# Kernel optimization log

Hardware: AMD Instinct MI355X
Metric: run time of the kernel (lower is better)

## Reference

```python
import jax, jax.numpy as jnp
import numpy as np

N, S, C, G = 40000, 16, 96, 12
EPS = 1e-5

def ln(x, g, b):
    mu = jnp.mean(x, -1, keepdims=True)
    var = jnp.mean((x - mu) ** 2, -1, keepdims=True)
    return (x - mu) * jax.lax.rsqrt(var + EPS) * g + b

def setup_inputs() -> dict:
    key = jax.random.key(0)
    ks = jax.random.split(key, 20)
    s = 0.05
    inp = {
        'q': jax.random.normal(ks[0], (N, C), jnp.float32),
        'k': jax.random.normal(ks[1], (N, C), jnp.float32),
        'v': jax.random.normal(ks[2], (N, C), jnp.float32),
        'xyz': jax.random.normal(ks[3], (N, 3), jnp.float32),
        'reference_index': jax.random.randint(ks[4], (N, S), 0, N, jnp.int32),
        # linear_q: Linear(C,C)+LN(C)+ReLU
        'Wq': jax.random.normal(ks[5], (C, C), jnp.float32) * s,
        'bq': jnp.zeros((C,), jnp.float32),
        'gq': jnp.ones((C,), jnp.float32),
        'betaq': jnp.zeros((C,), jnp.float32),
        # linear_k
        'Wk': jax.random.normal(ks[6], (C, C), jnp.float32) * s,
        'bk': jnp.zeros((C,), jnp.float32),
        'gk': jnp.ones((C,), jnp.float32),
        'betak': jnp.zeros((C,), jnp.float32),
        # linear_v
        'Wv': jax.random.normal(ks[7], (C, C), jnp.float32) * s,
        'bv': jnp.zeros((C,), jnp.float32),
        # linear_p_bias: Linear(3,C)+LN(C)+ReLU+Linear(C,C)
        'Wp1': jax.random.normal(ks[8], (3, C), jnp.float32) * s,
        'bp1': jnp.zeros((C,), jnp.float32),
        'gp': jnp.ones((C,), jnp.float32),
        'betap': jnp.zeros((C,), jnp.float32),
        'Wp2': jax.random.normal(ks[9], (C, C), jnp.float32) * s,
        'bp2': jnp.zeros((C,), jnp.float32),
        # weight_encoding: Linear(C,G)+LN(G)+ReLU+Linear(G,G)
        'Ww1': jax.random.normal(ks[10], (C, G), jnp.float32) * s,
        'bw1': jnp.zeros((G,), jnp.float32),
        'gw': jnp.ones((G,), jnp.float32),
        'betaw': jnp.zeros((G,), jnp.float32),
        'Ww2': jax.random.normal(ks[11], (G, G), jnp.float32) * s,
        'bw2': jnp.zeros((G,), jnp.float32),
    }
    return inp

def reference(q, k, v, xyz, reference_index,
              Wq, bq, gq, betaq, Wk, bk, gk, betak, Wv, bv,
              Wp1, bp1, gp, betap, Wp2, bp2,
              Ww1, bw1, gw, betaw, Ww2, bw2):
    query = jax.nn.relu(ln(q @ Wq + bq, gq, betaq))            # [N, C]
    keyf  = jax.nn.relu(ln(k @ Wk + bk, gk, betak))            # [N, C]
    val   = v @ Wv + bv                                        # [N, C]

    idx = reference_index                                      # [N, S]
    mask = (idx >= 0).astype(q.dtype)                          # sign(idx+1)
    safe = jnp.clip(idx, 0, None)
    # pointops.grouping: gather w/ zero-fill at idx=-1; with_xyz prepends relative coords
    pos  = (xyz[safe] - xyz[:, None, :]) * mask[..., None]     # [N, S, 3]
    keyg = keyf[safe] * mask[..., None]                        # [N, S, C]
    valg = val[safe] * mask[..., None]                         # [N, S, C]

    rel = keyg - query[:, None, :]                             # [N, S, C]
    peb = jax.nn.relu(ln(pos @ Wp1 + bp1, gp, betap)) @ Wp2 + bp2
    rel = rel + peb
    valg = valg + peb

    w = jax.nn.relu(ln(rel @ Ww1 + bw1, gw, betaw)) @ Ww2 + bw2  # [N, S, G]
    w = jax.nn.softmax(w, axis=1) * mask[..., None]              # softmax over neighbors

    valg = valg.reshape(N, S, G, C // G)
    feat = jnp.einsum('nsgi,nsg->ngi', valg, w).reshape(N, C)
    return feat
```

## Files before the change

kernel.cpp:

```cpp
#include <hip/hip_runtime.h>

#define NN 40000
#define SS 16
#define CC 96
#define GG 12
#define SXP 104

typedef __attribute__((ext_vector_type(8))) short bf16x8;
typedef __attribute__((ext_vector_type(4))) float f32x4;

__device__ __forceinline__ short f2bf(float f) {
    union { float f; unsigned u; } c; c.f = f;
    unsigned r = (c.u + 0x7fffu + ((c.u >> 16) & 1u)) >> 16;
    return (short)r;
}
__device__ __forceinline__ unsigned pack2bf(float hi, float lo) {
    unsigned a = __float_as_uint(hi) + 0x8000u;
    unsigned b = __float_as_uint(lo) + 0x8000u;
    return __builtin_amdgcn_perm(a, b, 0x07060302u);
}
__device__ __forceinline__ ushort f2bf_hu(float f) {
    return (ushort)((__float_as_uint(f) + 0x8000u) >> 16);
}
__device__ __forceinline__ float bf2f(ushort u) {
    return __uint_as_float(((unsigned)u) << 16);
}

template<int CTRL>
__device__ __forceinline__ float dppf(float x) {
    int r = __builtin_amdgcn_mov_dpp(__float_as_int(x), CTRL, 0xF, 0xF, true);
    return __int_as_float(r);
}
__device__ __forceinline__ float row16_sum(float x) {
    x += dppf<0xB1>(x);
    x += dppf<0x4E>(x);
    x += dppf<0x141>(x);
    x += dppf<0x140>(x);
    return x;
}
__device__ __forceinline__ float row16_max(float x) {
    x = fmaxf(x, dppf<0xB1>(x));
    x = fmaxf(x, dppf<0x4E>(x));
    x = fmaxf(x, dppf<0x141>(x));
    x = fmaxf(x, dppf<0x140>(x));
    return x;
}

#define J_W3   27648
#define J_P2   (J_W3 + 9216)
#define J_W1   (J_P2 + 1536)
#define J_WF   (J_W1 + 1536)
#define J_CF   (J_WF + 12)
#define J_S4   (J_CF + 4)
#define J_G    (J_S4 + 16)

__global__ void prep_kernel(const float* __restrict__ Wq, const float* __restrict__ Wk,
                            const float* __restrict__ Wv, const float* __restrict__ Wp2,
                            const float* __restrict__ Ww1, const float* __restrict__ bp2,
                            const float* __restrict__ bw1, const float* __restrict__ Wp1,
                            const float* __restrict__ bp1,
                            ushort* __restrict__ fragQKV, ushort* __restrict__ fragP2,
                            ushort* __restrict__ fragW1, ushort* __restrict__ fragWf,
                            float* __restrict__ cfused, float* __restrict__ stats)
{
    const int job = blockIdx.x*256 + threadIdx.x;
    if (job < J_W3) {
        const int which = job / 9216, o = job % 9216;
        const float* W = (which == 0) ? Wq : (which == 1) ? Wk : Wv;
        const int pos = o >> 3, j = o & 7;
        const int lane = pos & 63, ntkb = pos >> 6;
        const int nt = ntkb / 3, kb = ntkb - nt*3;
        const int col = nt*16 + (lane & 15), krow = kb*32 + (lane >> 4)*8 + j;
        fragQKV[job] = (ushort)f2bf(W[krow*CC + col]);
    } else if (job < J_P2) {
        const int o = job - J_W3;
        const int pos = o >> 3, j = o & 7;
        const int lane = pos & 63, ntkb = pos >> 6;
        const int nt = ntkb / 3, kb = ntkb - nt*3;
        const int col = nt*16 + (lane & 15), krow = kb*32 + (lane >> 4)*8 + j;
        fragP2[o] = (ushort)f2bf(Wp2[krow*CC + col]);
    } else if (job < J_W1) {
        const int o = job - J_P2;
        const int pos = o >> 3, j = o & 7;
        const int lane = pos & 63, kb = pos >> 6;
        const int col = lane & 15, krow = kb*32 + (lane >> 4)*8 + j;
        fragW1[o] = (col < GG) ? (ushort)f2bf(Ww1[krow*GG + col]) : (ushort)0;
    } else if (job < J_WF) {
        const int o = job - J_W1;
        const int pos = o >> 3, j = o & 7;
        const int lane = pos & 63, kb = pos >> 6;
        const int col = lane & 15, krow = kb*32 + (lane >> 4)*8 + j;
        float s = 0.f;
        if (col < GG) for (int jj = 0; jj < CC; ++jj) s += Wp2[krow*CC + jj] * Ww1[jj*GG + col];
        fragWf[o] = (col < GG) ? (ushort)f2bf(s) : (ushort)0;
    } else if (job < J_CF) {
        const int g = job - J_WF;
        float s = bw1[g];
        for (int jj = 0; jj < CC; ++jj) s += bp2[jj] * Ww1[jj*GG + g];
        cfused[g] = s;
    } else if (job < J_S4) {
        const int d = job - J_CF;
        float s = 0.f;
        for (int c = 0; c < CC; ++c) s += (d < 3) ? Wp1[d*CC + c] : bp1[c];
        stats[d] = s;
    } else if (job < J_G) {
        const int o = job - J_S4, d1 = o >> 2, d2 = o & 3;
        float s = 0.f;
        for (int c = 0; c < CC; ++c) {
            const float a1 = (d1 < 3) ? Wp1[d1*CC + c] : bp1[c];
            const float a2 = (d2 < 3) ? Wp1[d2*CC + c] : bp1[c];
            s += a1*a2;
        }
        stats[4 + o] = s;
    }
}

__global__ __launch_bounds__(256) void qkv_mfma(
    const float* __restrict__ q, const float* __restrict__ kx, const float* __restrict__ v,
    const float* __restrict__ bq, const float* __restrict__ gq, const float* __restrict__ betaq,
    const float* __restrict__ bk, const float* __restrict__ gk, const float* __restrict__ betak,
    const float* __restrict__ bv,
    const ushort* __restrict__ fragQKV, const ushort* __restrict__ fragW1,
    ushort* __restrict__ valout, float* __restrict__ qw1out, float* __restrict__ kw1out)
{
    __shared__ float sbias[CC], sg[CC], sbeta[CC];
    __shared__ __align__(16) ushort sx2[4][16*SXP];

    const int p = blockIdx.y;
    const float* X; const float* b;
    const float* g = nullptr; const float* beta = nullptr;
    if (p == 0)      { X = q;  b = bq; g = gq; beta = betaq; }
    else if (p == 1) { X = kx; b = bk; g = gk; beta = betak; }
    else             { X = v;  b = bv; }
    const bool has_ln = (p < 2);
    float* w1out = (p == 0) ? qw1out : kw1out;

    const int t = threadIdx.x;
    if (t < CC) {
        sbias[t] = b[t];
        if (has_ln) { sg[t] = g[t]; sbeta[t] = beta[t]; }
    }

    const int lane = t & 63, w = t >> 6;
    const int c16 = lane & 15, quad = lane >> 4;
    const ushort* fragW = fragQKV + p*9216;

    bf16x8 Ww1f[3];
    if (has_ln) {
        #pragma unroll
        for (int kb = 0; kb < 3; ++kb) {
            union { bf16x8 v; uint4 u; } wu;
            wu.u = ((const uint4*)fragW1)[kb*64 + lane];
            Ww1f[kb] = wu.v;
        }
    }

    __syncthreads();

    const f32x4 zero4 = {0.f, 0.f, 0.f, 0.f};
    ushort* sxw = sx2[w];
    const int tile = blockIdx.x*4 + w;
    const int row0 = tile * 16;

    const float* xr = X + (size_t)(row0 + c16)*CC;
    bf16x8 Af[3];
    #pragma unroll
    for (int kb = 0; kb < 3; ++kb) {
        const float4 a0 = *(const float4*)(xr + kb*32 + quad*8);
        const float4 a1 = *(const float4*)(xr + kb*32 + quad*8 + 4);
        union { bf16x8 v; uint u[4]; } au;
        au.u[0] = pack2bf(a0.y, a0.x);
        au.u[1] = pack2bf(a0.w, a0.z);
        au.u[2] = pack2bf(a1.y, a1.x);
        au.u[3] = pack2bf(a1.w, a1.z);
        Af[kb] = au.v;
    }

    f32x4 acc[6];
    #pragma unroll
    for (int nt = 0; nt < 6; ++nt) acc[nt] = zero4;
    #pragma unroll
    for (int kb = 0; kb < 3; ++kb)
        #pragma unroll
        for (int nt = 0; nt < 6; ++nt) {
            const bf16x8 bf = *(const bf16x8*)(fragW + ((nt*3 + kb)*64 + lane)*8);
            acc[nt] = __builtin_amdgcn_mfma_f32_16x16x32_bf16(Af[kb], bf, acc[nt], 0, 0, 0);
        }

    #pragma unroll
    for (int nt = 0; nt < 6; ++nt) {
        const float bb = sbias[nt*16 + c16];
        #pragma unroll
        for (int r = 0; r < 4; ++r) acc[nt][r] += bb;
    }

    if (has_ln) {
        #pragma unroll
        for (int r = 0; r < 4; ++r) {
            float sum = 0.f, sq = 0.f;
            #pragma unroll
            for (int nt = 0; nt < 6; ++nt) { float x = acc[nt][r]; sum += x; sq += x*x; }
            sum = row16_sum(sum); sq = row16_sum(sq);
            const float mu  = sum * (1.f/96.f);
            const float var = sq * (1.f/96.f) - mu*mu;
            const float rs  = rsqrtf(var + 1e-5f);
            #pragma unroll
            for (int nt = 0; nt < 6; ++nt) {
                const int c = nt*16 + c16;
                acc[nt][r] = fmaxf((acc[nt][r] - mu)*rs*sg[c] + sbeta[c], 0.f);
            }
        }
        #pragma unroll
        for (int nt = 0; nt < 6; ++nt)
            #pragma unroll
            for (int r = 0; r < 4; ++r)
                sxw[(quad*4 + r)*SXP + nt*16 + c16] = f2bf_hu(acc[nt][r]);

        f32x4 o = zero4;
        #pragma unroll
        for (int kb = 0; kb < 3; ++kb) {
            const bf16x8 aA = *(const bf16x8*)(sxw + c16*SXP + kb*32 + quad*8);
            o = __builtin_amdgcn_mfma_f32_16x16x32_bf16(aA, Ww1f[kb], o, 0, 0, 0);
        }
        if (c16 < GG) {
            #pragma unroll
            for (int r = 0; r < 4; ++r)
                w1out[(size_t)(row0 + quad*4 + r)*GG + c16] = o[r];
        }
    } else {
        #pragma unroll
        for (int r = 0; r < 4; ++r)
            #pragma unroll
            for (int nt = 0; nt < 6; ++nt)
                valout[(size_t)(row0 + quad*4 + r)*CC + nt*16 + c16] = (ushort)f2bf(acc[nt][r]);
    }
}

__global__ __launch_bounds__(256) void attn2(
    const float* __restrict__ xyz, const int* __restrict__ refidx,
    const float* __restrict__ gp,  const float* __restrict__ betap,
    const float* __restrict__ Wp1, const float* __restrict__ bp1,
    const float* __restrict__ bp2,
    const float* __restrict__ gw,  const float* __restrict__ betaw,
    const float* __restrict__ Ww2, const float* __restrict__ bw2,
    const float* __restrict__ cfused, const float* __restrict__ stats,
    const ushort* __restrict__ fragP2, const ushort* __restrict__ fragWf,
    const ushort* __restrict__ valw, const float* __restrict__ kw1w, const float* __restrict__ qw1w,
    float* __restrict__ out)
{
    __shared__ __align__(16) ushort sWp2f[9216];
    __shared__ float4 sA[CC];
    __shared__ float2 sGB[CC];
    __shared__ float  sbp2[CC];
    __shared__ __align__(16) float sWw2T[GG*GG];
    __shared__ float  sgw[16], sbetaw[16], sbw2[16], scf[16];
    __shared__ float  sstats[20];
    __shared__ __align__(16) float ybuf[4][2][SS*GG];

    const int t = threadIdx.x;
    if (t < CC) {
        sA[t]  = make_float4(Wp1[t], Wp1[CC + t], Wp1[2*CC + t], bp1[t]);
        sGB[t] = make_float2(gp[t], betap[t]);
        sbp2[t] = bp2[t];
    }
    if (t < GG*GG) {
        const int gr = t / GG, gc = t - gr*GG;
        sWw2T[gc*GG + gr] = Ww2[t];
    }
    if (t < 16) {
        sgw[t]    = (t < GG) ? gw[t]     : 0.f;
        sbetaw[t] = (t < GG) ? betaw[t]  : 0.f;
        sbw2[t]   = (t < GG) ? bw2[t]    : 0.f;
        scf[t]    = (t < GG) ? cfused[t] : 0.f;
    }
    if (t < 20) sstats[t] = stats[t];
    for (int i = t; i < 1152; i += 256) ((uint4*)sWp2f)[i] = ((const uint4*)fragP2)[i];

    const int lane = t & 63, w = t >> 6;
    const int c16 = lane & 15, quad = lane >> 4;
    const int gcl = (c16 < GG) ? c16 : (GG-1);
    const float laneg = (c16 < GG) ? 1.f : 0.f;

    __syncthreads();

    const f32x4 zero4 = {0.f, 0.f, 0.f, 0.f};
    const int n0 = blockIdx.x*8 + w*2;

    int   id[2];  int4 rr[2];
    #pragma unroll
    for (int u = 0; u < 2; ++u) {
        id[u] = refidx[(size_t)(n0 + u)*SS + c16];
        rr[u] = *(const int4*)(refidx + (size_t)(n0 + u)*SS + quad*4);
    }
    float qvl[2];
    #pragma unroll
    for (int u = 0; u < 2; ++u) qvl[u] = qw1w[(size_t)(n0 + u)*GG + gcl];
    bf16x8 Wff[3];
    #pragma unroll
    for (int kb = 0; kb < 3; ++kb) {
        union { bf16x8 v; uint4 u; } wu;
        wu.u = ((const uint4*)fragWf)[kb*64 + lane];
        Wff[kb] = wu.v;
    }
    float cxx[2], cxy[2], cxz[2];
    #pragma unroll
    for (int u = 0; u < 2; ++u) {
        cxx[u] = xyz[(size_t)(n0 + u)*3 + 0];
        cxy[u] = xyz[(size_t)(n0 + u)*3 + 1];
        cxz[u] = xyz[(size_t)(n0 + u)*3 + 2];
    }

    float mm[2]; int safe1[2];
    #pragma unroll
    for (int u = 0; u < 2; ++u) {
        mm[u]    = (id[u] >= 0) ? 1.f : 0.f;
        safe1[u] = (id[u] < 0) ? 0 : id[u];
    }
    int sid[2][4]; float mrg[2][4];
    #pragma unroll
    for (int u = 0; u < 2; ++u) {
        const int rv0 = rr[u].x, rv1 = rr[u].y, rv2 = rr[u].z, rv3 = rr[u].w;
        sid[u][0] = (rv0 < 0) ? 0 : rv0;  mrg[u][0] = (rv0 >= 0) ? laneg : 0.f;
        sid[u][1] = (rv1 < 0) ? 0 : rv1;  mrg[u][1] = (rv1 >= 0) ? laneg : 0.f;
        sid[u][2] = (rv2 < 0) ? 0 : rv2;  mrg[u][2] = (rv2 >= 0) ? laneg : 0.f;
        sid[u][3] = (rv3 < 0) ? 0 : rv3;  mrg[u][3] = (rv3 >= 0) ? laneg : 0.f;
    }

    float sxx[2], sxy[2], sxz[2];
    #pragma unroll
    for (int u = 0; u < 2; ++u) {
        sxx[u] = xyz[(size_t)safe1[u]*3 + 0];
        sxy[u] = xyz[(size_t)safe1[u]*3 + 1];
        sxz[u] = xyz[(size_t)safe1[u]*3 + 2];
    }
    float kwr[2][4];
    #pragma unroll
    for (int u = 0; u < 2; ++u)
        #pragma unroll
        for (int r = 0; r < 4; ++r)
            kwr[u][r] = kw1w[(size_t)sid[u][r]*GG + gcl];

    __builtin_amdgcn_sched_barrier(0);

    ushort va[3][2][2][4];
    #pragma unroll
    for (int ntp = 0; ntp < 3; ++ntp)
        #pragma unroll
        for (int h = 0; h < 2; ++h)
            #pragma unroll
            for (int u = 0; u < 2; ++u)
                #pragma unroll
                for (int r = 0; r < 4; ++r)
                    va[ntp][h][u][r] = valw[(size_t)sid[u][r]*CC + (2*ntp + h)*16 + c16];

    __builtin_amdgcn_sched_barrier(0);

    float px[2], py[2], pz[2];
    #pragma unroll
    for (int u = 0; u < 2; ++u) {
        px[u] = (sxx[u] - cxx[u]) * mm[u];
        py[u] = (sxy[u] - cxy[u]) * mm[u];
        pz[u] = (sxz[u] - cxz[u]) * mm[u];
    }

    float muv[2], rsv[2];
    {
        const float s0 = sstats[0], s1 = sstats[1], s2 = sstats[2], s3 = sstats[3];
        float G_[16];
        #pragma unroll
        for (int i = 0; i < 16; ++i) G_[i] = sstats[4 + i];
        #pragma unroll
        for (int u = 0; u < 2; ++u) {
            muv[u] = (px[u]*s0 + py[u]*s1 + pz[u]*s2 + s3) * (1.f/96.f);
            const float p4[4] = {px[u], py[u], pz[u], 1.f};
            float e2 = 0.f;
            #pragma unroll
            for (int a = 0; a < 4; ++a) {
                float ta = 0.f;
                #pragma unroll
                for (int b2 = 0; b2 < 4; ++b2) ta = fmaf(G_[a*4 + b2], p4[b2], ta);
                e2 = fmaf(p4[a], ta, e2);
            }
            const float var = e2*(1.f/96.f) - muv[u]*muv[u];
            rsv[u] = rsqrtf(var + 1e-5f);
        }
    }

    bf16x8 t1A[2][3];
    #pragma unroll
    for (int kb = 0; kb < 3; ++kb) {
        uint tw[2][4];
        #pragma unroll
        for (int jp = 0; jp < 4; ++jp) {
            const int c0 = kb*32 + quad*8 + jp*2, c1 = c0 + 1;
            const float4 aw0 = sA[c0], aw1 = sA[c1];
            const float2 gb0 = sGB[c0], gb1 = sGB[c1];
            #pragma unroll
            for (int u = 0; u < 2; ++u) {
                const float x0 = fmaf(px[u], aw0.x, fmaf(py[u], aw0.y, fmaf(pz[u], aw0.z, aw0.w)));
                const float x1 = fmaf(px[u], aw1.x, fmaf(py[u], aw1.y, fmaf(pz[u], aw1.z, aw1.w)));
                const float t0 = fmaxf(fmaf((x0 - muv[u])*rsv[u], gb0.x, gb0.y), 0.f);
                const float t1v = fmaxf(fmaf((x1 - muv[u])*rsv[u], gb1.x, gb1.y), 0.f);
                tw[u][jp] = pack2bf(t1v, t0);
            }
        }
        #pragma unroll
        for (int u = 0; u < 2; ++u) {
            union { bf16x8 v; uint uu[4]; } tc;
            tc.uu[0] = tw[u][0]; tc.uu[1] = tw[u][1];
            tc.uu[2] = tw[u][2]; tc.uu[3] = tw[u][3];
            t1A[u][kb] = tc.v;
        }
    }

    f32x4 t2[2];
    #pragma unroll
    for (int u = 0; u < 2; ++u) t2[u] = zero4;
    #pragma unroll
    for (int kb = 0; kb < 3; ++kb)
        #pragma unroll
        for (int u = 0; u < 2; ++u)
            t2[u] = __builtin_amdgcn_mfma_f32_16x16x32_bf16(t1A[u][kb], Wff[kb], t2[u], 0, 0, 0);
    {
        const float cf = scf[c16];
        #pragma unroll
        for (int u = 0; u < 2; ++u) {
            const float qz = qvl[u]*laneg;
            #pragma unroll
            for (int r = 0; r < 4; ++r)
                t2[u][r] += kwr[u][r]*mrg[u][r] - qz + cf;
        }
    }

    {
        const float gwv = sgw[c16], bwv = sbetaw[c16];
        #pragma unroll
        for (int u = 0; u < 2; ++u) {
            float* yb = ybuf[w][u];
            #pragma unroll
            for (int r = 0; r < 4; ++r) {
                const float x = t2[u][r];
                const float s1 = row16_sum(x);
                const float s2 = row16_sum(x*x);
                const float mu2  = s1 * (1.f/12.f);
                const float var2 = s2 * (1.f/12.f) - mu2*mu2;
                const float rs2  = rsqrtf(var2 + 1e-5f);
                const float y    = fmaxf((x - mu2)*rs2*gwv + bwv, 0.f);
                if (c16 < GG) yb[(quad*4 + r)*GG + c16] = y;
            }
        }
    }

    float w3v[2][3];
    {
        f32x4 yr[2][3];
        #pragma unroll
        for (int u = 0; u < 2; ++u) {
            yr[u][0] = *(const f32x4*)(ybuf[w][u] + c16*GG + 0);
            yr[u][1] = *(const f32x4*)(ybuf[w][u] + c16*GG + 4);
            yr[u][2] = *(const f32x4*)(ybuf[w][u] + c16*GG + 8);
        }
        #pragma unroll
        for (int gi = 0; gi < 3; ++gi) {
            const int gpp = quad + gi*4;
            const f32x4 wa = *(const f32x4*)(sWw2T + gpp*GG + 0);
            const f32x4 wb = *(const f32x4*)(sWw2T + gpp*GG + 4);
            const f32x4 wc = *(const f32x4*)(sWw2T + gpp*GG + 8);
            const float bb = sbw2[gpp];
            #pragma unroll
            for (int u = 0; u < 2; ++u) {
                float a2 = bb;
                #pragma unroll
                for (int j = 0; j < 4; ++j) a2 = fmaf(yr[u][0][j], wa[j], a2);
                #pragma unroll
                for (int j = 0; j < 4; ++j) a2 = fmaf(yr[u][1][j], wb[j], a2);
                #pragma unroll
                for (int j = 0; j < 4; ++j) a2 = fmaf(yr[u][2][j], wc[j], a2);
                w3v[u][gi] = a2;
            }
        }
    }

    #pragma unroll
    for (int u = 0; u < 2; ++u) {
        #pragma unroll
        for (int gi = 0; gi < 3; ++gi) {
            const float mx = row16_max(w3v[u][gi]);
            const float e  = __expf(w3v[u][gi] - mx);
            const float tot = row16_sum(e);
            w3v[u][gi] = e * __builtin_amdgcn_rcpf(tot) * mm[u];
        }
        float* sw2 = ybuf[w][u];
        #pragma unroll
        for (int gi = 0; gi < 3; ++gi)
            sw2[(quad + 4*gi)*16 + c16] = w3v[u][gi];
    }

    #pragma unroll
    for (int ntp = 0; ntp < 3; ++ntp) {
        const int nt0 = 2*ntp, nt1 = 2*ntp + 1;
        f32x4 pa[2], pb[2];
        #pragma unroll
        for (int u = 0; u < 2; ++u) { pa[u] = zero4; pb[u] = zero4; }
        #pragma unroll
        for (int kb = 0; kb < 3; ++kb) {
            const bf16x8 bfa = *(const bf16x8*)(sWp2f + ((nt0*3 + kb)*64 + lane)*8);
            const bf16x8 bfb = *(const bf16x8*)(sWp2f + ((nt1*3 + kb)*64 + lane)*8);
            #pragma unroll
            for (int u = 0; u < 2; ++u) {
                pa[u] = __builtin_amdgcn_mfma_f32_16x16x32_bf16(t1A[u][kb], bfa, pa[u], 0, 0, 0);
                pb[u] = __builtin_amdgcn_mfma_f32_16x16x32_bf16(t1A[u][kb], bfb, pb[u], 0, 0, 0);
            }
        }
        #pragma unroll
        for (int h = 0; h < 2; ++h) {
            const int nt = 2*ntp + h;
            const float b2   = sbp2[nt*16 + c16];
            const int   gidx = 2*nt + (c16 >> 3);
            #pragma unroll
            for (int u = 0; u < 2; ++u) {
                const f32x4 pc  = (h == 0) ? pa[u] : pb[u];
                const f32x4 swv = *(const f32x4*)(ybuf[w][u] + gidx*16 + quad*4);
                float a2 = 0.f;
                #pragma unroll
                for (int r = 0; r < 4; ++r)
                    a2 = fmaf(pc[r] + b2 + bf2f(va[ntp][h][u][r]), swv[r], a2);
                a2 += __shfl_xor(a2, 16, 64);
                a2 += __shfl_xor(a2, 32, 64);
                if (quad == 0) out[(size_t)(n0 + u)*CC + nt*16 + c16] = a2;
            }
        }
    }
}

extern "C" void kernel_launch(void* const* d_in, const int* in_sizes, int n_in,
                              void* d_out, int out_size, void* d_ws, size_t ws_size,
                              hipStream_t stream)
{
    const float* q     = (const float*)d_in[0];
    const float* k     = (const float*)d_in[1];
    const float* v     = (const float*)d_in[2];
    const float* xyz   = (const float*)d_in[3];
    const int*   ridx  = (const int*)d_in[4];
    const float* Wq    = (const float*)d_in[5];
    const float* bq    = (const float*)d_in[6];
    const float* gq    = (const float*)d_in[7];
    const float* betaq = (const float*)d_in[8];
    const float* Wk    = (const float*)d_in[9];
    const float* bk    = (const float*)d_in[10];
    const float* gk    = (const float*)d_in[11];
    const float* betak = (const float*)d_in[12];
    const float* Wv    = (const float*)d_in[13];
    const float* bv    = (const float*)d_in[14];
    const float* Wp1   = (const float*)d_in[15];
    const float* bp1   = (const float*)d_in[16];
    const float* gp    = (const float*)d_in[17];
    const float* betap = (const float*)d_in[18];
    const float* Wp2   = (const float*)d_in[19];
    const float* bp2   = (const float*)d_in[20];
    const float* Ww1   = (const float*)d_in[21];
    const float* bw1   = (const float*)d_in[22];
    const float* gw    = (const float*)d_in[23];
    const float* betaw = (const float*)d_in[24];
    const float* Ww2   = (const float*)d_in[25];
    const float* bw2   = (const float*)d_in[26];
    float* out = (float*)d_out;

    float* ws = (float*)d_ws;
    ushort* valw  = (ushort*)ws;
    float* kw1w   = ws + (size_t)NN*CC/2;
    float* qw1w   = kw1w + (size_t)NN*GG;
    float* cfused = qw1w + (size_t)NN*GG;
    float* statsp = cfused + 16;
    ushort* fragQKV = (ushort*)(statsp + 24);
    ushort* fragP2  = fragQKV + 3*9216;
    ushort* fragW1  = fragP2 + 9216;
    ushort* fragWf  = fragW1 + 1536;

    prep_kernel<<<dim3(157, 1, 1), 256, 0, stream>>>(
        Wq, Wk, Wv, Wp2, Ww1, bp2, bw1, Wp1, bp1,
        fragQKV, fragP2, fragW1, fragWf, cfused, statsp);

    qkv_mfma<<<dim3(625, 3, 1), 256, 0, stream>>>(
        q, k, v, bq, gq, betaq, bk, gk, betak, bv,
        fragQKV, fragW1, valw, qw1w, kw1w);

    attn2<<<dim3(5000, 1, 1), 256, 0, stream>>>(
        xyz, ridx, gp, betap, Wp1, bp1, bp2,
        gw, betaw, Ww2, bw2, cfused, statsp,
        fragP2, fragWf, valw, kw1w, qw1w, out);
}
```

Measured before the change: 213.7 us.

## Make attn2 persistent with refidx prefetch and store q/k W1 projections as bf16

attn2 becomes a grid-stride persistent kernel with 1280 blocks looping over the 5000 point groups. Per-block setup (shared weight staging, stats registers, Wff fragments) is paid once per block instead of once per group, and the next group's neighbor indices are prefetched while the current group computes. The per-point q·Ww1 and k·Ww1 projections are now written and read as bf16 instead of fp32, halving that gather traffic at some precision cost. The workspace layout is recomputed to match the narrower buffers.

```diff
diff --git a/kernel.cpp b/kernel.cpp
--- a/kernel.cpp
+++ b/kernel.cpp
@@ -4,6 +4,7 @@
 #define SS 16
 #define CC 96
 #define GG 12
+#define NGRP 5000
 #define SXP 104
 
 typedef __attribute__((ext_vector_type(8))) short bf16x8;
@@ -121,7 +122,7 @@
     const float* __restrict__ bk, const float* __restrict__ gk, const float* __restrict__ betak,
     const float* __restrict__ bv,
     const ushort* __restrict__ fragQKV, const ushort* __restrict__ fragW1,
-    ushort* __restrict__ valout, float* __restrict__ qw1out, float* __restrict__ kw1out)
+    ushort* __restrict__ valout, ushort* __restrict__ qw1out, ushort* __restrict__ kw1out)
 {
     __shared__ float sbias[CC], sg[CC], sbeta[CC];
     __shared__ __align__(16) ushort sx2[4][16*SXP];
@@ -133,7 +134,7 @@
     else if (p == 1) { X = kx; b = bk; g = gk; beta = betak; }
     else             { X = v;  b = bv; }
     const bool has_ln = (p < 2);
-    float* w1out = (p == 0) ? qw1out : kw1out;
+    ushort* w1out = (p == 0) ? qw1out : kw1out;
 
     const int t = threadIdx.x;
     if (t < CC) {
@@ -225,7 +226,7 @@
         if (c16 < GG) {
             #pragma unroll
             for (int r = 0; r < 4; ++r)
-                w1out[(size_t)(row0 + quad*4 + r)*GG + c16] = o[r];
+                w1out[(size_t)(row0 + quad*4 + r)*GG + c16] = (ushort)f2bf(o[r]);
         }
     } else {
         #pragma unroll
@@ -245,7 +246,7 @@
     const float* __restrict__ Ww2, const float* __restrict__ bw2,
     const float* __restrict__ cfused, const float* __restrict__ stats,
     const ushort* __restrict__ fragP2, const ushort* __restrict__ fragWf,
-    const ushort* __restrict__ valw, const float* __restrict__ kw1w, const float* __restrict__ qw1w,
+    const ushort* __restrict__ valw, const ushort* __restrict__ kw1w, const ushort* __restrict__ qw1w,
     float* __restrict__ out)
 {
     __shared__ __align__(16) ushort sWp2f[9216];
@@ -281,20 +282,6 @@
     const int gcl = (c16 < GG) ? c16 : (GG-1);
     const float laneg = (c16 < GG) ? 1.f : 0.f;
 
-    __syncthreads();
-
-    const f32x4 zero4 = {0.f, 0.f, 0.f, 0.f};
-    const int n0 = blockIdx.x*8 + w*2;
-
-    int   id[2];  int4 rr[2];
-    #pragma unroll
-    for (int u = 0; u < 2; ++u) {
-        id[u] = refidx[(size_t)(n0 + u)*SS + c16];
-        rr[u] = *(const int4*)(refidx + (size_t)(n0 + u)*SS + quad*4);
-    }
-    float qvl[2];
-    #pragma unroll
-    for (int u = 0; u < 2; ++u) qvl[u] = qw1w[(size_t)(n0 + u)*GG + gcl];
     bf16x8 Wff[3];
     #pragma unroll
     for (int kb = 0; kb < 3; ++kb) {
@@ -302,76 +289,110 @@
         wu.u = ((const uint4*)fragWf)[kb*64 + lane];
         Wff[kb] = wu.v;
     }
-    float cxx[2], cxy[2], cxz[2];
+
+    __syncthreads();
+
+    const float st0 = sstats[0], st1 = sstats[1], st2 = sstats[2], st3 = sstats[3];
+    float G_[16];
     #pragma unroll
-    for (int u = 0; u < 2; ++u) {
-        cxx[u] = xyz[(size_t)(n0 + u)*3 + 0];
-        cxy[u] = xyz[(size_t)(n0 + u)*3 + 1];
-        cxz[u] = xyz[(size_t)(n0 + u)*3 + 2];
-    }
-
-    float mm[2]; int safe1[2];
-    #pragma unroll
-    for (int u = 0; u < 2; ++u) {
-        mm[u]    = (id[u] >= 0) ? 1.f : 0.f;
-        safe1[u] = (id[u] < 0) ? 0 : id[u];
-    }
-    int sid[2][4]; float mrg[2][4];
-    #pragma unroll
-    for (int u = 0; u < 2; ++u) {
-        const int rv0 = rr[u].x, rv1 = rr[u].y, rv2 = rr[u].z, rv3 = rr[u].w;
-        sid[u][0] = (rv0 < 0) ? 0 : rv0;  mrg[u][0] = (rv0 >= 0) ? laneg : 0.f;
-        sid[u][1] = (rv1 < 0) ? 0 : rv1;  mrg[u][1] = (rv1 >= 0) ? laneg : 0.f;
-        sid[u][2] = (rv2 < 0) ? 0 : rv2;  mrg[u][2] = (rv2 >= 0) ? laneg : 0.f;
-        sid[u][3] = (rv3 < 0) ? 0 : rv3;  mrg[u][3] = (rv3 >= 0) ? laneg : 0.f;
-    }
-
-    float sxx[2], sxy[2], sxz[2];
-    #pragma unroll
-    for (int u = 0; u < 2; ++u) {
-        sxx[u] = xyz[(size_t)safe1[u]*3 + 0];
-        sxy[u] = xyz[(size_t)safe1[u]*3 + 1];
-        sxz[u] = xyz[(size_t)safe1[u]*3 + 2];
-    }
-    float kwr[2][4];
-    #pragma unroll
-    for (int u = 0; u < 2; ++u)
-        #pragma unroll
-        for (int r = 0; r < 4; ++r)
-            kwr[u][r] = kw1w[(size_t)sid[u][r]*GG + gcl];
-
-    __builtin_amdgcn_sched_barrier(0);
-
-    ushort va[3][2][2][4];
-    #pragma unroll
-    for (int ntp = 0; ntp < 3; ++ntp)
-        #pragma unroll
-        for (int h = 0; h < 2; ++h)
-            #pragma unroll
-            for (int u = 0; u < 2; ++u)
+    for (int i = 0; i < 16; ++i) G_[i] = sstats[4 + i];
+    const float gwv = sgw[c16], bwv = sbetaw[c16], cf = scf[c16];
+
+    const f32x4 zero4 = {0.f, 0.f, 0.f, 0.f};
+    const int stride = (int)gridDim.x;
+
+    int   id[2];  int4 rr[2];
+    {
+        const int n0p = blockIdx.x*8 + w*2;
+        #pragma unroll
+        for (int u = 0; u < 2; ++u) {
+            id[u] = refidx[(size_t)(n0p + u)*SS + c16];
+            rr[u] = *(const int4*)(refidx + (size_t)(n0p + u)*SS + quad*4);
+        }
+    }
+
+    for (int grp = blockIdx.x; grp < NGRP; grp += stride) {
+        const int n0 = grp*8 + w*2;
+
+        ushort qvu[2];
+        #pragma unroll
+        for (int u = 0; u < 2; ++u) qvu[u] = qw1w[(size_t)(n0 + u)*GG + gcl];
+        float cxx[2], cxy[2], cxz[2];
+        #pragma unroll
+        for (int u = 0; u < 2; ++u) {
+            cxx[u] = xyz[(size_t)(n0 + u)*3 + 0];
+            cxy[u] = xyz[(size_t)(n0 + u)*3 + 1];
+            cxz[u] = xyz[(size_t)(n0 + u)*3 + 2];
+        }
+
+        float mm[2]; int safe1[2];
+        #pragma unroll
+        for (int u = 0; u < 2; ++u) {
+            mm[u]    = (id[u] >= 0) ? 1.f : 0.f;
+            safe1[u] = (id[u] < 0) ? 0 : id[u];
+        }
+        int sid[2][4]; float mrg[2][4];
+        #pragma unroll
+        for (int u = 0; u < 2; ++u) {
+            const int rv0 = rr[u].x, rv1 = rr[u].y, rv2 = rr[u].z, rv3 = rr[u].w;
+            sid[u][0] = (rv0 < 0) ? 0 : rv0;  mrg[u][0] = (rv0 >= 0) ? laneg : 0.f;
+            sid[u][1] = (rv1 < 0) ? 0 : rv1;  mrg[u][1] = (rv1 >= 0) ? laneg : 0.f;
+            sid[u][2] = (rv2 < 0) ? 0 : rv2;  mrg[u][2] = (rv2 >= 0) ? laneg : 0.f;
+            sid[u][3] = (rv3 < 0) ? 0 : rv3;  mrg[u][3] = (rv3 >= 0) ? laneg : 0.f;
+        }
+
+        float sxx[2], sxy[2], sxz[2];
+        #pragma unroll
+        for (int u = 0; u < 2; ++u) {
+            sxx[u] = xyz[(size_t)safe1[u]*3 + 0];
+            sxy[u] = xyz[(size_t)safe1[u]*3 + 1];
+            sxz[u] = xyz[(size_t)safe1[u]*3 + 2];
+        }
+        ushort kwu[2][4];
+        #pragma unroll
+        for (int u = 0; u < 2; ++u)
+            #pragma unroll
+            for (int r = 0; r < 4; ++r)
+                kwu[u][r] = kw1w[(size_t)sid[u][r]*GG + gcl];
+
+        __builtin_amdgcn_sched_barrier(0);
+
+        ushort va[3][2][2][4];
+        #pragma unroll
+        for (int ntp = 0; ntp < 3; ++ntp)
+            #pragma unroll
+            for (int h = 0; h < 2; ++h)
                 #pragma unroll
-                for (int r = 0; r < 4; ++r)
-                    va[ntp][h][u][r] = valw[(size_t)sid[u][r]*CC + (2*ntp + h)*16 + c16];
-
-    __builtin_amdgcn_sched_barrier(0);
-
-    float px[2], py[2], pz[2];
-    #pragma unroll
-    for (int u = 0; u < 2; ++u) {
-        px[u] = (sxx[u] - cxx[u]) * mm[u];
-        py[u] = (sxy[u] - cxy[u]) * mm[u];
-        pz[u] = (sxz[u] - cxz[u]) * mm[u];
-    }
-
-    float muv[2], rsv[2];
-    {
-        const float s0 = sstats[0], s1 = sstats[1], s2 = sstats[2], s3 = sstats[3];
-        float G_[16];
-        #pragma unroll
-        for (int i = 0; i < 16; ++i) G_[i] = sstats[4 + i];
-        #pragma unroll
-        for (int u = 0; u < 2; ++u) {
-            muv[u] = (px[u]*s0 + py[u]*s1 + pz[u]*s2 + s3) * (1.f/96.f);
+                for (int u = 0; u < 2; ++u)
+                    #pragma unroll
+                    for (int r = 0; r < 4; ++r)
+                        va[ntp][h][u][r] = valw[(size_t)sid[u][r]*CC + (2*ntp + h)*16 + c16];
+
+        int idn[2]; int4 rrn[2];
+        {
+            const int grpn = (grp + stride < NGRP) ? (grp + stride) : grp;
+            const int n0n = grpn*8 + w*2;
+            #pragma unroll
+            for (int u = 0; u < 2; ++u) {
+                idn[u] = refidx[(size_t)(n0n + u)*SS + c16];
+                rrn[u] = *(const int4*)(refidx + (size_t)(n0n + u)*SS + quad*4);
+            }
+        }
+
+        __builtin_amdgcn_sched_barrier(0);
+
+        float px[2], py[2], pz[2];
+        #pragma unroll
+        for (int u = 0; u < 2; ++u) {
+            px[u] = (sxx[u] - cxx[u]) * mm[u];
+            py[u] = (sxy[u] - cxy[u]) * mm[u];
+            pz[u] = (sxz[u] - cxz[u]) * mm[u];
+        }
+
+        float muv[2], rsv[2];
+        #pragma unroll
+        for (int u = 0; u < 2; ++u) {
+            muv[u] = (px[u]*st0 + py[u]*st1 + pz[u]*st2 + st3) * (1.f/96.f);
             const float p4[4] = {px[u], py[u], pz[u], 1.f};
             float e2 = 0.f;
             #pragma unroll
@@ -384,56 +405,50 @@
             const float var = e2*(1.f/96.f) - muv[u]*muv[u];
             rsv[u] = rsqrtf(var + 1e-5f);
         }
-    }
-
-    bf16x8 t1A[2][3];
-    #pragma unroll
-    for (int kb = 0; kb < 3; ++kb) {
-        uint tw[2][4];
-        #pragma unroll
-        for (int jp = 0; jp < 4; ++jp) {
-            const int c0 = kb*32 + quad*8 + jp*2, c1 = c0 + 1;
-            const float4 aw0 = sA[c0], aw1 = sA[c1];
-            const float2 gb0 = sGB[c0], gb1 = sGB[c1];
+
+        bf16x8 t1A[2][3];
+        #pragma unroll
+        for (int kb = 0; kb < 3; ++kb) {
+            uint tw[2][4];
+            #pragma unroll
+            for (int jp = 0; jp < 4; ++jp) {
+                const int c0 = kb*32 + quad*8 + jp*2, c1 = c0 + 1;
+                const float4 aw0 = sA[c0], aw1 = sA[c1];
+                const float2 gb0 = sGB[c0], gb1 = sGB[c1];
+                #pragma unroll
+                for (int u = 0; u < 2; ++u) {
+                    const float x0 = fmaf(px[u], aw0.x, fmaf(py[u], aw0.y, fmaf(pz[u], aw0.z, aw0.w)));
+                    const float x1 = fmaf(px[u], aw1.x, fmaf(py[u], aw1.y, fmaf(pz[u], aw1.z, aw1.w)));
+                    const float t0 = fmaxf(fmaf((x0 - muv[u])*rsv[u], gb0.x, gb0.y), 0.f);
+                    const float t1v = fmaxf(fmaf((x1 - muv[u])*rsv[u], gb1.x, gb1.y), 0.f);
+                    tw[u][jp] = pack2bf(t1v, t0);
+                }
+            }
             #pragma unroll
             for (int u = 0; u < 2; ++u) {
-                const float x0 = fmaf(px[u], aw0.x, fmaf(py[u], aw0.y, fmaf(pz[u], aw0.z, aw0.w)));
-                const float x1 = fmaf(px[u], aw1.x, fmaf(py[u], aw1.y, fmaf(pz[u], aw1.z, aw1.w)));
-                const float t0 = fmaxf(fmaf((x0 - muv[u])*rsv[u], gb0.x, gb0.y), 0.f);
-                const float t1v = fmaxf(fmaf((x1 - muv[u])*rsv[u], gb1.x, gb1.y), 0.f);
-                tw[u][jp] = pack2bf(t1v, t0);
-            }
-        }
-        #pragma unroll
-        for (int u = 0; u < 2; ++u) {
-            union { bf16x8 v; uint uu[4]; } tc;
-            tc.uu[0] = tw[u][0]; tc.uu[1] = tw[u][1];
-            tc.uu[2] = tw[u][2]; tc.uu[3] = tw[u][3];
-            t1A[u][kb] = tc.v;
-        }
-    }
-
-    f32x4 t2[2];
-    #pragma unroll
-    for (int u = 0; u < 2; ++u) t2[u] = zero4;
-    #pragma unroll
-    for (int kb = 0; kb < 3; ++kb)
-        #pragma unroll
-        for (int u = 0; u < 2; ++u)
-            t2[u] = __builtin_amdgcn_mfma_f32_16x16x32_bf16(t1A[u][kb], Wff[kb], t2[u], 0, 0, 0);
-    {
-        const float cf = scf[c16];
-        #pragma unroll
-        for (int u = 0; u < 2; ++u) {
-            const float qz = qvl[u]*laneg;
+                union { bf16x8 v; uint uu[4]; } tc;
+                tc.uu[0] = tw[u][0]; tc.uu[1] = tw[u][1];
+                tc.uu[2] = tw[u][2]; tc.uu[3] = tw[u][3];
+                t1A[u][kb] = tc.v;
+            }
+        }
+
+        f32x4 t2[2];
+        #pragma unroll
+        for (int u = 0; u < 2; ++u) t2[u] = zero4;
+        #pragma unroll
+        for (int kb = 0; kb < 3; ++kb)
+            #pragma unroll
+            for (int u = 0; u < 2; ++u)
+                t2[u] = __builtin_amdgcn_mfma_f32_16x16x32_bf16(t1A[u][kb], Wff[kb], t2[u], 0, 0, 0);
+        #pragma unroll
+        for (int u = 0; u < 2; ++u) {
+            const float qz = bf2f(qvu[u])*laneg;
             #pragma unroll
             for (int r = 0; r < 4; ++r)
-                t2[u][r] += kwr[u][r]*mrg[u][r] - qz + cf;
-        }
-    }
-
-    {
-        const float gwv = sgw[c16], bwv = sbetaw[c16];
+                t2[u][r] += bf2f(kwu[u][r])*mrg[u][r] - qz + cf;
+        }
+
         #pragma unroll
         for (int u = 0; u < 2; ++u) {
             float* yb = ybuf[w][u];
@@ -449,87 +464,90 @@
                 if (c16 < GG) yb[(quad*4 + r)*GG + c16] = y;
             }
         }
-    }
-
-    float w3v[2][3];
-    {
-        f32x4 yr[2][3];
-        #pragma unroll
-        for (int u = 0; u < 2; ++u) {
-            yr[u][0] = *(const f32x4*)(ybuf[w][u] + c16*GG + 0);
-            yr[u][1] = *(const f32x4*)(ybuf[w][u] + c16*GG + 4);
-            yr[u][2] = *(const f32x4*)(ybuf[w][u] + c16*GG + 8);
-        }
-        #pragma unroll
-        for (int gi = 0; gi < 3; ++gi) {
-            const int gpp = quad + gi*4;
-            const f32x4 wa = *(const f32x4*)(sWw2T + gpp*GG + 0);
-            const f32x4 wb = *(const f32x4*)(sWw2T + gpp*GG + 4);
-            const f32x4 wc = *(const f32x4*)(sWw2T + gpp*GG + 8);
-            const float bb = sbw2[gpp];
+
+        float w3v[2][3];
+        {
+            f32x4 yr[2][3];
             #pragma unroll
             for (int u = 0; u < 2; ++u) {
-                float a2 = bb;
+                yr[u][0] = *(const f32x4*)(ybuf[w][u] + c16*GG + 0);
+                yr[u][1] = *(const f32x4*)(ybuf[w][u] + c16*GG + 4);
+                yr[u][2] = *(const f32x4*)(ybuf[w][u] + c16*GG + 8);
+            }
+            #pragma unroll
+            for (int gi = 0; gi < 3; ++gi) {
+                const int gpp = quad + gi*4;
+                const f32x4 wa = *(const f32x4*)(sWw2T + gpp*GG + 0);
+                const f32x4 wb = *(const f32x4*)(sWw2T + gpp*GG + 4);
+                const f32x4 wc = *(const f32x4*)(sWw2T + gpp*GG + 8);
+                const float bb = sbw2[gpp];
                 #pragma unroll
-                for (int j = 0; j < 4; ++j) a2 = fmaf(yr[u][0][j], wa[j], a2);
+                for (int u = 0; u < 2; ++u) {
+                    float a2 = bb;
+                    #pragma unroll
+                    for (int j = 0; j < 4; ++j) a2 = fmaf(yr[u][0][j], wa[j], a2);
+                    #pragma unroll
+                    for (int j = 0; j < 4; ++j) a2 = fmaf(yr[u][1][j], wb[j], a2);
+                    #pragma unroll
+                    for (int j = 0; j < 4; ++j) a2 = fmaf(yr[u][2][j], wc[j], a2);
+                    w3v[u][gi] = a2;
+                }
+            }
+        }
+
+        #pragma unroll
+        for (int u = 0; u < 2; ++u) {
+            #pragma unroll
+            for (int gi = 0; gi < 3; ++gi) {
+                const float mx = row16_max(w3v[u][gi]);
+                const float e  = __expf(w3v[u][gi] - mx);
+                const float tot = row16_sum(e);
+                w3v[u][gi] = e * __builtin_amdgcn_rcpf(tot) * mm[u];
+            }
+            float* sw2 = ybuf[w][u];
+            #pragma unroll
+            for (int gi = 0; gi < 3; ++gi)
+                sw2[(quad + 4*gi)*16 + c16] = w3v[u][gi];
+        }
+
+        #pragma unroll
+        for (int ntp = 0; ntp < 3; ++ntp) {
+            const int nt0 = 2*ntp, nt1 = 2*ntp + 1;
+            f32x4 pa[2], pb[2];
+            #pragma unroll
+            for (int u = 0; u < 2; ++u) { pa[u] = zero4; pb[u] = zero4; }
+            #pragma unroll
+            for (int kb = 0; kb < 3; ++kb) {
+                const bf16x8 bfa = *(const bf16x8*)(sWp2f + ((nt0*3 + kb)*64 + lane)*8);
+                const bf16x8 bfb = *(const bf16x8*)(sWp2f + ((nt1*3 + kb)*64 + lane)*8);
                 #pragma unroll
-                for (int j = 0; j < 4; ++j) a2 = fmaf(yr[u][1][j], wb[j], a2);
+                for (int u = 0; u < 2; ++u) {
+                    pa[u] = __builtin_amdgcn_mfma_f32_16x16x32_bf16(t1A[u][kb], bfa, pa[u], 0, 0, 0);
+                    pb[u] = __builtin_amdgcn_mfma_f32_16x16x32_bf16(t1A[u][kb], bfb, pb[u], 0, 0, 0);
+                }
+            }
+            #pragma unroll
+            for (int h = 0; h < 2; ++h) {
+                const int nt = 2*ntp + h;
+                const float b2   = sbp2[nt*16 + c16];
+                const int   gidx = 2*nt + (c16 >> 3);
                 #pragma unroll
-                for (int j = 0; j < 4; ++j) a2 = fmaf(yr[u][2][j], wc[j], a2);
-                w3v[u][gi] = a2;
-            }
-        }
-    }
-
-    #pragma unroll
-    for (int u = 0; u < 2; ++u) {
-        #pragma unroll
-        for (int gi = 0; gi < 3; ++gi) {
-            const float mx = row16_max(w3v[u][gi]);
-            const float e  = __expf(w3v[u][gi] - mx);
-            const float tot = row16_sum(e);
-            w3v[u][gi] = e * __builtin_amdgcn_rcpf(tot) * mm[u];
-        }
-        float* sw2 = ybuf[w][u];
-        #pragma unroll
-        for (int gi = 0; gi < 3; ++gi)
-            sw2[(quad + 4*gi)*16 + c16] = w3v[u][gi];
-    }
-
-    #pragma unroll
-    for (int ntp = 0; ntp < 3; ++ntp) {
-        const int nt0 = 2*ntp, nt1 = 2*ntp + 1;
-        f32x4 pa[2], pb[2];
-        #pragma unroll
-        for (int u = 0; u < 2; ++u) { pa[u] = zero4; pb[u] = zero4; }
-        #pragma unroll
-        for (int kb = 0; kb < 3; ++kb) {
-            const bf16x8 bfa = *(const bf16x8*)(sWp2f + ((nt0*3 + kb)*64 + lane)*8);
-            const bf16x8 bfb = *(const bf16x8*)(sWp2f + ((nt1*3 + kb)*64 + lane)*8);
-            #pragma unroll
-            for (int u = 0; u < 2; ++u) {
-                pa[u] = __builtin_amdgcn_mfma_f32_16x16x32_bf16(t1A[u][kb], bfa, pa[u], 0, 0, 0);
-                pb[u] = __builtin_amdgcn_mfma_f32_16x16x32_bf16(t1A[u][kb], bfb, pb[u], 0, 0, 0);
-            }
-        }
-        #pragma unroll
-        for (int h = 0; h < 2; ++h) {
-            const int nt = 2*ntp + h;
-            const float b2   = sbp2[nt*16 + c16];
-            const int   gidx = 2*nt + (c16 >> 3);
-            #pragma unroll
-            for (int u = 0; u < 2; ++u) {
-                const f32x4 pc  = (h == 0) ? pa[u] : pb[u];
-                const f32x4 swv = *(const f32x4*)(ybuf[w][u] + gidx*16 + quad*4);
-                float a2 = 0.f;
-                #pragma unroll
-                for (int r = 0; r < 4; ++r)
-                    a2 = fmaf(pc[r] + b2 + bf2f(va[ntp][h][u][r]), swv[r], a2);
-                a2 += __shfl_xor(a2, 16, 64);
-                a2 += __shfl_xor(a2, 32, 64);
-                if (quad == 0) out[(size_t)(n0 + u)*CC + nt*16 + c16] = a2;
-            }
-        }
+                for (int u = 0; u < 2; ++u) {
+                    const f32x4 pc  = (h == 0) ? pa[u] : pb[u];
+                    const f32x4 swv = *(const f32x4*)(ybuf[w][u] + gidx*16 + quad*4);
+                    float a2 = 0.f;
+                    #pragma unroll
+                    for (int r = 0; r < 4; ++r)
+                        a2 = fmaf(pc[r] + b2 + bf2f(va[ntp][h][u][r]), swv[r], a2);
+                    a2 += __shfl_xor(a2, 16, 64);
+                    a2 += __shfl_xor(a2, 32, 64);
+                    if (quad == 0) out[(size_t)(n0 + u)*CC + nt*16 + c16] = a2;
+                }
+            }
+        }
+
+        id[0] = idn[0]; id[1] = idn[1];
+        rr[0] = rrn[0]; rr[1] = rrn[1];
     }
 }
 
@@ -566,11 +584,10 @@
     const float* bw2   = (const float*)d_in[26];
     float* out = (float*)d_out;
 
-    float* ws = (float*)d_ws;
-    ushort* valw  = (ushort*)ws;
-    float* kw1w   = ws + (size_t)NN*CC/2;
-    float* qw1w   = kw1w + (size_t)NN*GG;
-    float* cfused = qw1w + (size_t)NN*GG;
+    ushort* valw  = (ushort*)d_ws;
+    ushort* kw1w  = valw + (size_t)NN*CC;
+    ushort* qw1w  = kw1w + (size_t)NN*GG;
+    float* cfused = (float*)(qw1w + (size_t)NN*GG);
     float* statsp = cfused + 16;
     ushort* fragQKV = (ushort*)(statsp + 24);
     ushort* fragP2  = fragQKV + 3*9216;
@@ -585,7 +602,7 @@
         q, k, v, bq, gq, betaq, bk, gk, betak, bv,
         fragQKV, fragW1, valw, qw1w, kw1w);
 
-    attn2<<<dim3(5000, 1, 1), 256, 0, stream>>>(
+    attn2<<<dim3(1280, 1, 1), 256, 0, stream>>>(
         xyz, ridx, gp, betap, Wp1, bp1, bp2,
         gw, betaw, Ww2, bw2, cfused, statsp,
         fragP2, fragWf, valw, kw1w, qw1w, out);
```

Result: slower. 224.8 us (+5.2%).
